# Performance work log

Measured on AMD Instinct MI355X. Metric: run time of the kernel, lower is better.

Reference implementation:

```python
import jax, jax.numpy as jnp
import numpy as np
import math

N, E, S, V, H, R = 10000, 160000, 512, 128, 8, 32
HD = S // H
CUTOFF = 10.0


def bessel_basis(d):
    # d: [E] -> [E, R], Bessel RBF with cosine cutoff
    freqs = jnp.arange(1, R + 1, dtype=d.dtype) * np.pi / CUTOFF  # [R]
    d1 = d[:, None]
    b = jnp.sin(freqs * d1) / jnp.maximum(d1, 1e-8)
    cut = 0.5 * (jnp.cos(np.pi * d1 / CUTOFF) + 1.0) * (d1 < CUTOFF).astype(d.dtype)
    return b * cut


def segment_softmax(logits, seg, num_seg):
    # logits: [E, H], seg: [E] destination node ids
    m = jax.ops.segment_max(logits, seg, num_segments=num_seg)
    m = jnp.where(jnp.isfinite(m), m, 0.0)
    e = jnp.exp(logits - m[seg])
    s = jax.ops.segment_sum(e, seg, num_segments=num_seg)
    return e / (s[seg] + 1e-9)


def layernorm(x, g, b, eps=1e-5):
    mu = jnp.mean(x, axis=-1, keepdims=True)
    var = jnp.mean(jnp.square(x - mu), axis=-1, keepdims=True)
    return (x - mu) * jax.lax.rsqrt(var + eps) * g + b


def setup_inputs() -> dict:
    key = jax.random.key(0)
    ks = jax.random.split(key, 24)
    sc = lambda fan_in: 1.0 / math.sqrt(fan_in)
    inp = {
        "scalars": jax.random.normal(ks[0], (N, S), jnp.float32),
        "vectors": jax.random.normal(ks[1], (N, V, 3), jnp.float32),
        "edge_vec": jax.random.normal(ks[2], (E, 3), jnp.float32),
        "Wq_s": jax.random.normal(ks[3], (S, S), jnp.float32) * sc(S),
        "bq_s": jnp.zeros((S,), jnp.float32),
        "Wk_s": jax.random.normal(ks[4], (S, S), jnp.float32) * sc(S),
        "bk_s": jnp.zeros((S,), jnp.float32),
        "Wv_s": jax.random.normal(ks[5], (S, S), jnp.float32) * sc(S),
        "bv_s": jnp.zeros((S,), jnp.float32),
        "Wq_v": jax.random.normal(ks[6], (V, V), jnp.float32) * sc(V),
        "Wk_v": jax.random.normal(ks[7], (V, V), jnp.float32) * sc(V),
        "Wv_v": jax.random.normal(ks[8], (V, V), jnp.float32) * sc(V),
        "Wout_s": jax.random.normal(ks[9], (S, S), jnp.float32) * sc(S),
        "bout_s": jnp.zeros((S,), jnp.float32),
        "Wout_v": jax.random.normal(ks[10], (V, V), jnp.float32) * sc(V),
        "bout_v": jnp.zeros((V,), jnp.float32),
        "W_edge": jax.random.normal(ks[11], (R, H), jnp.float32) * sc(R),
        "b_edge": jnp.zeros((H,), jnp.float32),
        "ln_g": jnp.ones((S,), jnp.float32),
        "ln_b": jnp.zeros((S,), jnp.float32),
        "edge_index": jax.random.randint(ks[12], (2, E), 0, N, jnp.int64),
    }
    return inp


def reference(scalars, vectors, edge_vec, Wq_s, bq_s, Wk_s, bk_s, Wv_s, bv_s,
              Wq_v, Wk_v, Wv_v, Wout_s, bout_s, Wout_v, bout_v,
              W_edge, b_edge, ln_g, ln_b, edge_index):
    row, col = edge_index[0], edge_index[1]
    edge_dist = jnp.linalg.norm(edge_vec, axis=-1)  # [E]

    # scalar Q/K/V, split into heads
    q_s = (scalars @ Wq_s + bq_s).reshape(N, H, HD)
    k_s = (scalars @ Wk_s + bk_s).reshape(N, H, HD)
    v_s = (scalars @ Wv_s + bv_s).reshape(N, H, HD)

    # vector Q/K/V: channel-mixing linear over the num_vectors axis (equivariant in 3D)
    q_v = jnp.einsum('nvi,vw->nwi', vectors, Wq_v)
    k_v = jnp.einsum('nvi,vw->nwi', vectors, Wk_v)
    v_v = jnp.einsum('nvi,vw->nwi', vectors, Wv_v)

    # per-edge attention logits
    att_s = jnp.einsum('ehd,ehd->eh', q_s[row], k_s[col])          # [E,H]
    att_v = jnp.einsum('evi,evi->e', q_v[row], k_v[col]) / math.sqrt(3.0)
    edge_att = bessel_basis(edge_dist) @ W_edge + b_edge            # [E,H]
    logits = (att_s + att_v[:, None] + edge_att) / math.sqrt(HD)

    # softmax over incoming edges of each destination node (row)
    attn = segment_softmax(logits, row, N)                          # [E,H]

    # scalar messages (per-head)
    msg_s = attn[:, :, None] * v_s[col]                             # [E,H,HD]
    out_s = jax.ops.segment_sum(msg_s, row, num_segments=N).reshape(N, S)
    out_s = out_s @ Wout_s + bout_s

    # vector messages (head-averaged attention, scalar gate keeps equivariance)
    a_v = jnp.mean(attn, axis=-1)                                   # [E]
    msg_v = a_v[:, None, None] * v_v[col]                           # [E,V,3]
    out_v = jax.ops.segment_sum(msg_v, row, num_segments=N)         # [N,V,3]
    out_v = jnp.einsum('nvi,vw->nwi', out_v, Wout_v) + bout_v[None, :, None]

    scalars_out = layernorm(scalars + out_s, ln_g, ln_b)
    vectors_out = vectors + out_v
    return scalars_out, vectors_out
```

## Files before the change

### kernel.cpp

```cpp
#include <hip/hip_runtime.h>
#include <math.h>

#define N_NODES 10000
#define E_EDGES 160000
#define S_DIM 512
#define QKV3 (3*S_DIM)
#define V_DIM 128
#define VQKV3 (3*V_DIM)
#define H_HEADS 8
#define R_BASIS 32
#define HD_DIM 64
#define NV3 (V_DIM*3)
#define KV8P 896

typedef _Float16 f16;
typedef f16 f16x2 __attribute__((ext_vector_type(2)));
typedef f16 f16x8 __attribute__((ext_vector_type(8)));
typedef float f32x4 __attribute__((ext_vector_type(4)));

static __device__ __forceinline__ float h2f(unsigned short u) {
  f16 h; __builtin_memcpy(&h, &u, 2); return (float)h;
}
static __device__ __forceinline__ unsigned short f2h(float f) {
  f16 h = (f16)f; unsigned short u; __builtin_memcpy(&u, &h, 2); return u;
}
static __device__ __forceinline__ float wave_max(float v) {
  #pragma unroll
  for (int o = 32; o > 0; o >>= 1) v = fmaxf(v, __shfl_xor(v, o, 64));
  return v;
}

#if defined(__has_builtin)
#if __has_builtin(__builtin_amdgcn_sdot4)
#define SDOT4(a, b, c) __builtin_amdgcn_sdot4((int)(a), (int)(b), (c), false)
#endif
#endif
#ifndef SDOT4
static __device__ __forceinline__ int sdot4_sw(unsigned int a, unsigned int b, int c) {
  #pragma unroll
  for (int j = 0; j < 4; ++j)
    c += (int)(char)((a >> (8 * j)) & 0xff) * (int)(char)((b >> (8 * j)) & 0xff);
  return c;
}
#define SDOT4(a, b, c) sdot4_sw((a), (b), (c))
#endif

static __device__ __forceinline__ void fma_i8x4(unsigned int w, float wt, float* acc) {
  acc[0] = fmaf(wt, (float)(int)(char)(w & 0xff), acc[0]);
  acc[1] = fmaf(wt, (float)(int)(char)((w >> 8) & 0xff), acc[1]);
  acc[2] = fmaf(wt, (float)(int)(char)((w >> 16) & 0xff), acc[2]);
  acc[3] = fmaf(wt, (float)(int)(char)((w >> 24) & 0xff), acc[3]);
}

static __device__ __forceinline__ void glds16(const unsigned short* g, unsigned short* l) {
  __builtin_amdgcn_global_load_lds(
      (const __attribute__((address_space(1))) unsigned int*)g,
      (__attribute__((address_space(3))) unsigned int*)l, 16, 0, 0);
}

__global__ __launch_bounds__(256) void prep_kernel(
    const float* __restrict__ scalars, unsigned short* __restrict__ Af16,
    const int* __restrict__ ei, int* __restrict__ counts,
    const float* __restrict__ bq, const float* __restrict__ bk,
    const float* __restrict__ bv, float* __restrict__ bias_cat)
{
  int b = blockIdx.x, t = threadIdx.x;
  if (b < 5000) {
    int i = b * 256 + t;
    float4 v = reinterpret_cast<const float4*>(scalars)[i];
    ushort4 o;
    o.x = f2h(v.x); o.y = f2h(v.y); o.z = f2h(v.z); o.w = f2h(v.w);
    reinterpret_cast<ushort4*>(Af16)[i] = o;
  } else if (b < 5625) {
    int e = (b - 5000) * 256 + t;
    if (e < E_EDGES) atomicAdd(&counts[ei[e]], 1);
  } else {
    int c = (b - 5625) * 256 + t;
    if (c < QKV3)
      bias_cat[c] = (c < 512) ? bq[c] : (c < 1024) ? bk[c - 512] : bv[c - 1024];
  }
}

__global__ __launch_bounds__(256) void transpose4_kernel(
    const float* __restrict__ W0, const float* __restrict__ W1,
    const float* __restrict__ W2, const float* __restrict__ W3,
    unsigned short* __restrict__ Dcat, unsigned short* __restrict__ Do, int D)
{
  __shared__ float t[32][33];
  int z = blockIdx.z;
  const float* W = (z == 0) ? W0 : (z == 1) ? W1 : (z == 2) ? W2 : W3;
  unsigned short* dst = (z < 3) ? Dcat + (size_t)z * D * D : Do;
  int n0 = blockIdx.x * 32, k0 = blockIdx.y * 32;
  int x = threadIdx.x, y = threadIdx.y;
  #pragma unroll
  for (int j = 0; j < 32; j += 8)
    t[y + j][x] = W[(size_t)(k0 + y + j) * D + n0 + x];
  __syncthreads();
  #pragma unroll
  for (int j = 0; j < 32; j += 8)
    dst[(size_t)(n0 + y + j) * D + k0 + x] = f2h(t[x][y + j]);
}

__global__ __launch_bounds__(128) void vec_transpose_kernel(
    const float* __restrict__ vecs, unsigned short* __restrict__ VT)
{
  __shared__ float l[NV3];
  int n = blockIdx.x, t = threadIdx.x;
  #pragma unroll
  for (int j = 0; j < 3; ++j) l[t + j * 128] = vecs[(size_t)n * NV3 + t + j * 128];
  __syncthreads();
  #pragma unroll
  for (int i = 0; i < 3; ++i)
    VT[((size_t)n * 3 + i) * V_DIM + t] = f2h(l[t * 3 + i]);
}

__global__ __launch_bounds__(256) void gemm_f16_kernel(
    const unsigned short* __restrict__ A, const unsigned short* __restrict__ Bt,
    const float* __restrict__ bias, float* __restrict__ Cf,
    unsigned short* __restrict__ Ch, int M, int K, int Nn)
{
  __shared__ unsigned short lds[2][2][128 * 32];
  int tid = threadIdx.x;
  int wid = tid >> 6, lane = tid & 63;
  int wr = wid >> 1, wc = wid & 1;
  int row0 = blockIdx.y * 128, col0 = blockIdx.x * 128;

  int r0 = tid >> 2, s0 = tid & 3;
  int r1 = r0 + 64;
  int sw0 = (r0 >> 1) & 3;
  int aoff = (s0 ^ sw0) * 8;
  int gra0 = row0 + r0; if (gra0 >= M) gra0 = M - 1;
  int gra1 = row0 + r1; if (gra1 >= M) gra1 = M - 1;
  const unsigned short* ag0 = A + (size_t)gra0 * K + aoff;
  const unsigned short* ag1 = A + (size_t)gra1 * K + aoff;
  const unsigned short* bg0 = Bt + (size_t)(col0 + r0) * K + aoff;
  const unsigned short* bg1 = Bt + (size_t)(col0 + r1) * K + aoff;

  f32x4 acc[4][4];
  #pragma unroll
  for (int m = 0; m < 4; ++m)
    #pragma unroll
    for (int n = 0; n < 4; ++n) acc[m][n] = (f32x4){0.f, 0.f, 0.f, 0.f};

  int lr = lane & 15, lq = lane >> 4;
  int slot = (lq ^ ((lr >> 1) & 3)) * 8;
  int aro[4], bro[4];
  #pragma unroll
  for (int m = 0; m < 4; ++m) aro[m] = (wr * 64 + m * 16 + lr) * 32 + slot;
  #pragma unroll
  for (int n = 0; n < 4; ++n) bro[n] = (wc * 64 + n * 16 + lr) * 32 + slot;

  int nk = K >> 5;
  glds16(ag0, &lds[0][0][tid * 8]);
  glds16(ag1, &lds[0][0][(tid + 256) * 8]);
  glds16(bg0, &lds[0][1][tid * 8]);
  glds16(bg1, &lds[0][1][(tid + 256) * 8]);
  __syncthreads();

  for (int t = 0; t < nk; ++t) {
    int cur = t & 1;
    if (t + 1 < nk) {
      int ko = (t + 1) << 5;
      glds16(ag0 + ko, &lds[cur ^ 1][0][tid * 8]);
      glds16(ag1 + ko, &lds[cur ^ 1][0][(tid + 256) * 8]);
      glds16(bg0 + ko, &lds[cur ^ 1][1][tid * 8]);
      glds16(bg1 + ko, &lds[cur ^ 1][1][(tid + 256) * 8]);
    }
    const unsigned short* Ab = lds[cur][0];
    const unsigned short* Bb = lds[cur][1];
    f16x8 af[4], bf[4];
    #pragma unroll
    for (int m = 0; m < 4; ++m) af[m] = *reinterpret_cast<const f16x8*>(Ab + aro[m]);
    #pragma unroll
    for (int n = 0; n < 4; ++n) bf[n] = *reinterpret_cast<const f16x8*>(Bb + bro[n]);
    #pragma unroll
    for (int m = 0; m < 4; ++m)
      #pragma unroll
      for (int n = 0; n < 4; ++n)
        acc[m][n] = __builtin_amdgcn_mfma_f32_16x16x32_f16(af[m], bf[n], acc[m][n], 0, 0, 0);
    __syncthreads();
  }

  float bcol[4];
  #pragma unroll
  for (int n = 0; n < 4; ++n)
    bcol[n] = bias ? bias[col0 + wc * 64 + n * 16 + lr] : 0.f;
  int rl = tid >> 3, cc = (tid & 7) * 16;

  if (Cf) {
    float* cst = reinterpret_cast<float*>(&lds[0][0][0]);
    #pragma unroll
    for (int m = 0; m < 4; ++m) {
      __syncthreads();
      #pragma unroll
      for (int n = 0; n < 4; ++n)
        #pragma unroll
        for (int j = 0; j < 4; ++j)
          cst[(wr * 16 + lq * 4 + j) * 128 + wc * 64 + n * 16 + lr] = acc[m][n][j] + bcol[n];
      __syncthreads();
      int row = row0 + (rl >> 4) * 64 + m * 16 + (rl & 15);
      if (row < M) {
        float4* dst = reinterpret_cast<float4*>(Cf + (size_t)row * Nn + col0 + cc);
        const float4* src = reinterpret_cast<const float4*>(cst + rl * 128 + cc);
        dst[0] = src[0]; dst[1] = src[1]; dst[2] = src[2]; dst[3] = src[3];
      }
    }
  } else {
    unsigned short* csth = &lds[0][0][0];
    #pragma unroll
    for (int m = 0; m < 4; ++m) {
      __syncthreads();
      #pragma unroll
      for (int n = 0; n < 4; ++n)
        #pragma unroll
        for (int j = 0; j < 4; ++j)
          csth[(wr * 16 + lq * 4 + j) * 128 + wc * 64 + n * 16 + lr] = f2h(acc[m][n][j] + bcol[n]);
      __syncthreads();
      int row = row0 + (rl >> 4) * 64 + m * 16 + (rl & 15);
      if (row < M) {
        int4* dst = reinterpret_cast<int4*>(Ch + (size_t)row * Nn + col0 + cc);
        const int4* src = reinterpret_cast<const int4*>(csth + rl * 128 + cc);
        dst[0] = src[0]; dst[1] = src[1];
      }
    }
  }
}

__global__ __launch_bounds__(256) void pack_i8_kernel(
    const unsigned short* __restrict__ qkv_s, const unsigned short* __restrict__ qkv_v,
    char* __restrict__ q8, char* __restrict__ k8, char* __restrict__ v8,
    float* __restrict__ scales)
{
  __shared__ float am[336];
  __shared__ float inv_sh[3];
  int n = blockIdx.x, t = threadIdx.x;
  float va[2][8];

  auto loadChunk = [&](int chunk, float* v) {
    int r = chunk / 112, j = chunk - r * 112;
    int c = j * 8;
    const unsigned short* src;
    if (c < 512) {
      src = qkv_s + (size_t)n * QKV3 + r * 512 + c;
    } else {
      int cc = c - 512, i = cc >> 7, w = cc & 127;
      src = qkv_v + ((size_t)n * 3 + i) * VQKV3 + r * 128 + w;
    }
    int4 sv = *reinterpret_cast<const int4*>(src);
    union { int4 x; unsigned short u[8]; } us; us.x = sv;
    float m = 0.f;
    #pragma unroll
    for (int q = 0; q < 8; ++q) { v[q] = h2f(us.u[q]); m = fmaxf(m, fabsf(v[q])); }
    am[chunk] = m;
  };

  loadChunk(t, va[0]);
  if (t < 80) loadChunk(256 + t, va[1]);
  __syncthreads();

  int lane = t & 63, wid = t >> 6;
  if (wid < 3) {
    int basec = wid * 112;
    float m = am[basec + lane];
    if (lane < 48) m = fmaxf(m, am[basec + 64 + lane]);
    m = wave_max(m);
    if (lane == 0) {
      m = fmaxf(m, 1e-8f);
      scales[3 * n + wid] = m * (1.f / 127.f);
      inv_sh[wid] = 127.f / m;
    }
  }
  __syncthreads();

  auto quantStore = [&](int chunk, const float* v) {
    int r = chunk / 112, j = chunk - r * 112;
    float inv = inv_sh[r];
    unsigned int b0 = 0, b1 = 0;
    #pragma unroll
    for (int q = 0; q < 4; ++q) {
      int x = __float2int_rn(v[q] * inv);
      b0 |= ((unsigned)(x & 0xff)) << (8 * q);
    }
    #pragma unroll
    for (int q = 0; q < 4; ++q) {
      int x = __float2int_rn(v[4 + q] * inv);
      b1 |= ((unsigned)(x & 0xff)) << (8 * q);
    }
    char* dst = (r == 0 ? q8 : r == 1 ? k8 : v8) + (size_t)n * KV8P + j * 8;
    uint2 o; o.x = b0; o.y = b1;
    *reinterpret_cast<uint2*>(dst) = o;
  };

  quantStore(t, va[0]);
  if (t < 80) quantStore(256 + t, va[1]);
}

__global__ __launch_bounds__(1024) void scan_kernel(const int* __restrict__ counts,
                                                    int* __restrict__ offs) {
  __shared__ int wsum[16];
  __shared__ int carry_s;
  int tid = threadIdx.x;
  int lane = tid & 63, w = tid >> 6;
  if (tid == 0) carry_s = 0;
  __syncthreads();
  for (int base = 0; base < N_NODES; base += 1024) {
    int i = base + tid;
    int v = (i < N_NODES) ? counts[i] : 0;
    int x = v;
    #pragma unroll
    for (int o = 1; o < 64; o <<= 1) {
      int t = __shfl_up(x, o, 64);
      if (lane >= o) x += t;
    }
    if (lane == 63) wsum[w] = x;
    __syncthreads();
    if (w == 0 && lane < 16) {
      int t = wsum[lane];
      #pragma unroll
      for (int o = 1; o < 16; o <<= 1) {
        int u = __shfl_up(t, o, 64);
        if (lane >= o) t += u;
      }
      wsum[lane] = t;
    }
    __syncthreads();
    int incl = x + ((w > 0) ? wsum[w - 1] : 0);
    int c = carry_s;
    __syncthreads();
    if (i < N_NODES) offs[i] = c + incl - v;
    if (tid == 1023) carry_s = c + incl;
    __syncthreads();
  }
  if (tid == 0) offs[N_NODES] = carry_s;
}

__global__ void scatter_kernel(const int* __restrict__ ei, const int* __restrict__ offs,
                               int* __restrict__ cursor, int* __restrict__ eord) {
  int e = blockIdx.x * 256 + threadIdx.x;
  if (e < E_EDGES) {
    int r = ei[e];
    int p = offs[r] + atomicAdd(&cursor[r], 1);
    eord[p] = e;
  }
}

#define MAXDEG 512
__global__ __launch_bounds__(256) void agg_fused_kernel(
    const char* __restrict__ q8, const char* __restrict__ k8,
    const char* __restrict__ v8, const float* __restrict__ scales,
    const float* __restrict__ edge_vec, const int* __restrict__ ei,
    const int* __restrict__ eord, const int* __restrict__ offs,
    const float* __restrict__ W_edge, const float* __restrict__ b_edge,
    unsigned short* __restrict__ out_s, unsigned short* __restrict__ out_v)
{
  __shared__ float attn_lds[MAXDEG * H_HEADS];
  __shared__ float av_lds[MAXDEG];
  __shared__ int col_lds[MAXDEG];
  __shared__ uint4 q_lds[56];
  __shared__ float Wl[R_BASIS * H_HEADS];
  __shared__ float m_sh[H_HEADS], inv_sh[H_HEADS];
  __shared__ float sq_sh;

  int n = blockIdx.x;
  int beg = offs[n];
  int deg = offs[n + 1] - beg;
  if (deg > MAXDEG) deg = MAXDEG;
  int tid = threadIdx.x;
  Wl[tid] = W_edge[tid];
  if (tid < 56) q_lds[tid] = reinterpret_cast<const uint4*>(q8 + (size_t)n * KV8P)[tid];
  if (tid == 56) sq_sh = scales[3 * n + 0];
  __syncthreads();

  int lane = tid & 63, wv = tid >> 6;
  int g = lane >> 3, h = lane & 7;
  float sq = sq_sh;

  for (int i = wv * 8 + g; i < deg; i += 32) {
    int e = eord[beg + i];
    int col = ei[E_EDGES + e];
    const char* kp = k8 + (size_t)col * KV8P;
    uint4 ka[4], kv[3];
    #pragma unroll
    for (int r = 0; r < 4; ++r)
      ka[r] = *reinterpret_cast<const uint4*>(kp + h * HD_DIM + r * 16);
    #pragma unroll
    for (int r = 0; r < 3; ++r)
      kv[r] = *reinterpret_cast<const uint4*>(kp + 512 + h * 48 + r * 16);
    float sk = scales[3 * col + 1];
    float ex = edge_vec[(size_t)e * 3 + 0];
    float ey = edge_vec[(size_t)e * 3 + 1];
    float ez = edge_vec[(size_t)e * 3 + 2];

    int dsum = 0;
    #pragma unroll
    for (int r = 0; r < 4; ++r) {
      uint4 qa = q_lds[h * 4 + r];
      dsum = SDOT4(qa.x, ka[r].x, dsum);
      dsum = SDOT4(qa.y, ka[r].y, dsum);
      dsum = SDOT4(qa.z, ka[r].z, dsum);
      dsum = SDOT4(qa.w, ka[r].w, dsum);
    }
    int dvec = 0;
    #pragma unroll
    for (int r = 0; r < 3; ++r) {
      uint4 qv = q_lds[32 + h * 3 + r];
      dvec = SDOT4(qv.x, kv[r].x, dvec);
      dvec = SDOT4(qv.y, kv[r].y, dvec);
      dvec = SDOT4(qv.z, kv[r].z, dvec);
      dvec = SDOT4(qv.w, kv[r].w, dvec);
    }
    dvec += __shfl_xor(dvec, 1, 64);
    dvec += __shfl_xor(dvec, 2, 64);
    dvec += __shfl_xor(dvec, 4, 64);
    float att = sq * sk * ((float)dsum + 0.57735026918962576f * (float)dvec);

    float d = sqrtf(ex * ex + ey * ey + ez * ez);
    float th = d * 0.31415926535897932f;
    float s1 = __sinf(th), c1 = __cosf(th);
    float s2 = 2.f * s1 * c1,         c2 = fmaf(c1, c1, -s1 * s1);
    float s3 = fmaf(s2, c1, c2 * s1), c3 = fmaf(c2, c1, -s2 * s1);
    float s4 = 2.f * s2 * c2,         c4 = fmaf(c2, c2, -s2 * s2);
    float sr[4] = {s1, s2, s3, s4};
    float cr[4] = {c1, c2, c3, c4};
    float acc = 0.f;
    #pragma unroll
    for (int t = 0; t < 8; ++t) {
      #pragma unroll
      for (int j = 0; j < 4; ++j) {
        acc = fmaf(sr[j], Wl[(t * 4 + j) * H_HEADS + h], acc);
        float sn = fmaf(sr[j], c4, cr[j] * s4);
        cr[j] = fmaf(cr[j], c4, -sr[j] * s4);
        sr[j] = sn;
      }
    }
    float cut = (d < 10.f) ? 0.5f * (c1 + 1.f) : 0.f;
    float eah = fmaf(acc, cut / fmaxf(d, 1e-8f), b_edge[h]);

    attn_lds[i * 8 + h] = (att + eah) * 0.125f;
    if (h == 0) col_lds[i] = col;
  }
  __syncthreads();

  if (wv == 0) {
    float m = -INFINITY;
    for (int i = g; i < deg; i += 8) m = fmaxf(m, attn_lds[i * 8 + h]);
    m = fmaxf(m, __shfl_xor(m, 8, 64));
    m = fmaxf(m, __shfl_xor(m, 16, 64));
    m = fmaxf(m, __shfl_xor(m, 32, 64));

    float s = 0.f;
    for (int i = g; i < deg; i += 8) {
      float w = __expf(attn_lds[i * 8 + h] - m);
      attn_lds[i * 8 + h] = w;
      s += w;
    }
    s += __shfl_xor(s, 8, 64);
    s += __shfl_xor(s, 16, 64);
    s += __shfl_xor(s, 32, 64);
    float inv = 1.f / (s + 1e-9f);
    if (lane < 8) { m_sh[lane] = m; inv_sh[lane] = inv; }

    for (int i = g; i < deg; i += 8) {
      float t = attn_lds[i * 8 + h] * inv;
      t += __shfl_xor(t, 1, 64);
      t += __shfl_xor(t, 2, 64);
      t += __shfl_xor(t, 4, 64);
      if (h == 0) av_lds[i] = 0.125f * t;
    }
  }
  __syncthreads();

  int hc = lane >> 3;
  float ih = inv_sh[hc];
  float accs[8] = {0,0,0,0,0,0,0,0};
  float accv[8] = {0,0,0,0,0,0,0,0};
  for (int i = wv; i < deg; i += 4) {
    int colv = col_lds[i];
    float svc = scales[3 * colv + 2];
    float wgt = attn_lds[i * 8 + hc] * ih * svc;
    float av = av_lds[i] * svc;
    uint2 vs = *reinterpret_cast<const uint2*>(v8 + (size_t)colv * KV8P + lane * 8);
    fma_i8x4(vs.x, wgt, accs);
    fma_i8x4(vs.y, wgt, accs + 4);
    if (lane < 48) {
      uint2 vvl = *reinterpret_cast<const uint2*>(v8 + (size_t)colv * KV8P + 512 + lane * 8);
      fma_i8x4(vvl.x, av, accv);
      fma_i8x4(vvl.y, av, accv + 4);
    }
  }
  __syncthreads();

  float* red_s = attn_lds;
  float* red_v = attn_lds + 2048;
  #pragma unroll
  for (int j = 0; j < 8; j += 4)
    *reinterpret_cast<float4*>(&red_s[wv * 512 + lane * 8 + j]) =
      make_float4(accs[j], accs[j+1], accs[j+2], accs[j+3]);
  if (lane < 48) {
    #pragma unroll
    for (int j = 0; j < 8; j += 4)
      *reinterpret_cast<float4*>(&red_v[wv * 384 + lane * 8 + j]) =
        make_float4(accv[j], accv[j+1], accv[j+2], accv[j+3]);
  }
  __syncthreads();

  {
    int d0 = 2 * tid;
    float s0 = red_s[d0] + red_s[512 + d0] + red_s[1024 + d0] + red_s[1536 + d0];
    float s1 = red_s[d0+1] + red_s[512 + d0+1] + red_s[1024 + d0+1] + red_s[1536 + d0+1];
    ushort2 o; o.x = f2h(s0); o.y = f2h(s1);
    *reinterpret_cast<ushort2*>(out_s + (size_t)n * S_DIM + d0) = o;
  }
  if (tid < 192) {
    int d0 = 2 * tid;
    float s0 = red_v[d0] + red_v[384 + d0] + red_v[768 + d0] + red_v[1152 + d0];
    float s1 = red_v[d0+1] + red_v[384 + d0+1] + red_v[768 + d0+1] + red_v[1152 + d0+1];
    ushort2 o; o.x = f2h(s0); o.y = f2h(s1);
    *reinterpret_cast<ushort2*>(out_v + (size_t)n * NV3 + d0) = o;
  }
}

__global__ __launch_bounds__(128) void vec_epilogue_kernel(
    const float* __restrict__ tmp, const float* __restrict__ bout_v,
    const float* __restrict__ vectors, float* __restrict__ out)
{
  __shared__ float l[NV3];
  int n = blockIdx.x, t = threadIdx.x;
  #pragma unroll
  for (int i = 0; i < 3; ++i)
    l[i * 128 + t] = tmp[((size_t)n * 3 + i) * V_DIM + t];
  __syncthreads();
  #pragma unroll
  for (int c = 0; c < 3; ++c) {
    int j = t + c * 128;
    int w = j / 3, i = j - 3 * w;
    out[(size_t)n * NV3 + j] = l[i * 128 + w] + bout_v[w] + vectors[(size_t)n * NV3 + j];
  }
}

__global__ __launch_bounds__(256) void ln_kernel(
    const float* __restrict__ x0, const float* __restrict__ dx,
    const float* __restrict__ g, const float* __restrict__ b,
    float* __restrict__ out)
{
  int r = blockIdx.x * 4 + (threadIdx.x >> 6);
  int lane = threadIdx.x & 63;
  if (r >= N_NODES) return;
  float x[8];
  float s = 0.f;
  #pragma unroll
  for (int j = 0; j < 8; ++j) {
    int d = lane + j * 64;
    x[j] = x0[(size_t)r * S_DIM + d] + dx[(size_t)r * S_DIM + d];
    s += x[j];
  }
  #pragma unroll
  for (int o = 32; o > 0; o >>= 1) s += __shfl_xor(s, o, 64);
  float mu = s * (1.f / 512.f);
  float vs = 0.f;
  #pragma unroll
  for (int j = 0; j < 8; ++j) { float t = x[j] - mu; vs += t * t; }
  #pragma unroll
  for (int o = 32; o > 0; o >>= 1) vs += __shfl_xor(vs, o, 64);
  float inv = rsqrtf(vs * (1.f / 512.f) + 1e-5f);
  #pragma unroll
  for (int j = 0; j < 8; ++j) {
    int d = lane + j * 64;
    out[(size_t)r * S_DIM + d] = (x[j] - mu) * inv * g[d] + b[d];
  }
}

extern "C" void kernel_launch(void* const* d_in, const int* in_sizes, int n_in,
                              void* d_out, int out_size, void* d_ws, size_t ws_size,
                              hipStream_t stream)
{
  (void)in_sizes; (void)n_in; (void)out_size; (void)ws_size;
  const float* scalars  = (const float*)d_in[0];
  const float* vectors  = (const float*)d_in[1];
  const float* edge_vec = (const float*)d_in[2];
  const float* Wq_s = (const float*)d_in[3];
  const float* bq_s = (const float*)d_in[4];
  const float* Wk_s = (const float*)d_in[5];
  const float* bk_s = (const float*)d_in[6];
  const float* Wv_s = (const float*)d_in[7];
  const float* bv_s = (const float*)d_in[8];
  const float* Wq_v = (const float*)d_in[9];
  const float* Wk_v = (const float*)d_in[10];
  const float* Wv_v = (const float*)d_in[11];
  const float* Wout_s = (const float*)d_in[12];
  const float* bout_s = (const float*)d_in[13];
  const float* Wout_v = (const float*)d_in[14];
  const float* bout_v = (const float*)d_in[15];
  const float* W_edge = (const float*)d_in[16];
  const float* b_edge = (const float*)d_in[17];
  const float* ln_g = (const float*)d_in[18];
  const float* ln_b = (const float*)d_in[19];
  const int* ei = (const int*)d_in[20];

  float* out = (float*)d_out;
  const size_t NS  = (size_t)N_NODES * S_DIM;
  const size_t NVs = (size_t)N_NODES * NV3;
  const size_t WSZ = (size_t)S_DIM * S_DIM;
  const size_t WVZ = (size_t)V_DIM * V_DIM;
  const int MV = N_NODES * 3;

  char* base = (char*)d_ws;
  auto carve = [&](size_t bytes) -> char* {
    char* p = base;
    base += (bytes + 255) & ~(size_t)255;
    return p;
  };
  unsigned short* Af16 = (unsigned short*)carve(NS * 2);
  unsigned short* VT0  = (unsigned short*)carve(NVs * 2);
  float* tmpv = (float*)Af16;
  char* v8 = (char*)Af16;
  unsigned short* qkv_s = (unsigned short*)carve((size_t)N_NODES * QKV3 * 2);
  unsigned short* qkv_v = (unsigned short*)carve((size_t)MV * VQKV3 * 2);
  unsigned short* outs_pre = (unsigned short*)carve(NS * 2);
  unsigned short* outv_pre = (unsigned short*)carve(NVs * 2);
  float* dx       = (float*)carve(NS * 4);
  char* q8 = (char*)dx;
  char* k8 = q8 + (size_t)N_NODES * KV8P;
  unsigned short* WqkvT  = (unsigned short*)carve(3 * WSZ * 2);
  unsigned short* WoT    = (unsigned short*)carve(WSZ * 2);
  unsigned short* WqkvvT = (unsigned short*)carve(3 * WVZ * 2);
  unsigned short* WovT   = (unsigned short*)carve(WVZ * 2);
  float* bias_cat = (float*)carve(QKV3 * 4);
  float* scales   = (float*)carve(3 * N_NODES * 4);
  int* counts = (int*)carve(N_NODES * 4);
  int* offs   = (int*)carve((N_NODES + 1) * 4);
  int* cursor = (int*)carve(N_NODES * 4);
  int* eord   = (int*)carve(E_EDGES * 4);

  hipMemsetAsync(counts, 0, N_NODES * sizeof(int), stream);
  hipMemsetAsync(cursor, 0, N_NODES * sizeof(int), stream);

  prep_kernel<<<5631, 256, 0, stream>>>(scalars, Af16, ei, counts,
                                        bq_s, bk_s, bv_s, bias_cat);
  dim3 tBlk(32, 8);
  transpose4_kernel<<<dim3(16, 16, 4), tBlk, 0, stream>>>(Wq_s, Wk_s, Wv_s, Wout_s, WqkvT, WoT, S_DIM);
  transpose4_kernel<<<dim3(4, 4, 4), tBlk, 0, stream>>>(Wq_v, Wk_v, Wv_v, Wout_v, WqkvvT, WovT, V_DIM);
  vec_transpose_kernel<<<N_NODES, 128, 0, stream>>>(vectors, VT0);

  gemm_f16_kernel<<<dim3(QKV3 / 128, (N_NODES + 127) / 128), 256, 0, stream>>>(
      Af16, WqkvT, bias_cat, nullptr, qkv_s, N_NODES, S_DIM, QKV3);
  gemm_f16_kernel<<<dim3(VQKV3 / 128, (MV + 127) / 128), 256, 0, stream>>>(
      VT0, WqkvvT, nullptr, nullptr, qkv_v, MV, V_DIM, VQKV3);

  pack_i8_kernel<<<N_NODES, 256, 0, stream>>>(qkv_s, qkv_v, q8, k8, v8, scales);

  scan_kernel<<<1, 1024, 0, stream>>>(counts, offs);
  scatter_kernel<<<(E_EDGES + 255) / 256, 256, 0, stream>>>(ei, offs, cursor, eord);

  agg_fused_kernel<<<N_NODES, 256, 0, stream>>>(q8, k8, v8, scales, edge_vec,
                                                ei, eord, offs, W_edge, b_edge,
                                                outs_pre, outv_pre);

  gemm_f16_kernel<<<dim3(S_DIM / 128, (N_NODES + 127) / 128), 256, 0, stream>>>(
      outs_pre, WoT, bout_s, dx, nullptr, N_NODES, S_DIM, S_DIM);
  gemm_f16_kernel<<<dim3(1, (MV + 127) / 128), 256, 0, stream>>>(
      outv_pre, WovT, nullptr, tmpv, nullptr, MV, V_DIM, V_DIM);
  vec_epilogue_kernel<<<N_NODES, 128, 0, stream>>>(tmpv, bout_v, vectors, out + NS);
  ln_kernel<<<2500, 256, 0, stream>>>(scalars, dx, ln_g, ln_b, out);
}
```

Before: 258.5 us.

## Split edge logits into column-bucketed pass for K-cache locality before aggregation

Moves the per-edge attention logit computation out of the per-node aggregation kernel into a separate persistent kernel. That kernel processes edges sorted into four source-column buckets so gathered K rows stay cache-resident, and it writes logits and columns in destination order. The aggregation kernel then only loads precomputed logits for the softmax and V accumulation, with a smaller degree cap and a 2x unrolled loop. This adds a second scan, extra atomics, an E×H float logits round trip through memory, and more launches. It also lowers MAXDEG from 512 to 128, which could truncate high-degree nodes.

```diff
diff --git a/kernel.cpp b/kernel.cpp
--- a/kernel.cpp
+++ b/kernel.cpp
@@ -12,9 +12,11 @@
 #define HD_DIM 64
 #define NV3 (V_DIM*3)
 #define KV8P 896
+#define NBKT 4
+#define BKT_DIV 2500
+#define NKEYS (NBKT * N_NODES)
 
 typedef _Float16 f16;
-typedef f16 f16x2 __attribute__((ext_vector_type(2)));
 typedef f16 f16x8 __attribute__((ext_vector_type(8)));
 typedef float f32x4 __attribute__((ext_vector_type(4)));
 
@@ -60,7 +62,7 @@
 
 __global__ __launch_bounds__(256) void prep_kernel(
     const float* __restrict__ scalars, unsigned short* __restrict__ Af16,
-    const int* __restrict__ ei, int* __restrict__ counts,
+    const int* __restrict__ ei, int* __restrict__ counts, int* __restrict__ bc,
     const float* __restrict__ bq, const float* __restrict__ bk,
     const float* __restrict__ bv, float* __restrict__ bias_cat)
 {
@@ -73,7 +75,11 @@
     reinterpret_cast<ushort4*>(Af16)[i] = o;
   } else if (b < 5625) {
     int e = (b - 5000) * 256 + t;
-    if (e < E_EDGES) atomicAdd(&counts[ei[e]], 1);
+    if (e < E_EDGES) {
+      int row = ei[e], col = ei[E_EDGES + e];
+      atomicAdd(&counts[row], 1);
+      atomicAdd(&bc[(col / BKT_DIV) * N_NODES + row], 1);
+    }
   } else {
     int c = (b - 5625) * 256 + t;
     if (c < QKV3)
@@ -296,16 +302,16 @@
 }
 
 __global__ __launch_bounds__(1024) void scan_kernel(const int* __restrict__ counts,
-                                                    int* __restrict__ offs) {
+                                                    int* __restrict__ offs, int n) {
   __shared__ int wsum[16];
   __shared__ int carry_s;
   int tid = threadIdx.x;
   int lane = tid & 63, w = tid >> 6;
   if (tid == 0) carry_s = 0;
   __syncthreads();
-  for (int base = 0; base < N_NODES; base += 1024) {
+  for (int base = 0; base < n; base += 1024) {
     int i = base + tid;
-    int v = (i < N_NODES) ? counts[i] : 0;
+    int v = (i < n) ? counts[i] : 0;
     int x = v;
     #pragma unroll
     for (int o = 1; o < 64; o <<= 1) {
@@ -327,131 +333,162 @@
     int incl = x + ((w > 0) ? wsum[w - 1] : 0);
     int c = carry_s;
     __syncthreads();
-    if (i < N_NODES) offs[i] = c + incl - v;
+    if (i < n) offs[i] = c + incl - v;
     if (tid == 1023) carry_s = c + incl;
     __syncthreads();
   }
-  if (tid == 0) offs[N_NODES] = carry_s;
-}
-
-__global__ void scatter_kernel(const int* __restrict__ ei, const int* __restrict__ offs,
-                               int* __restrict__ cursor, int* __restrict__ eord) {
+  if (tid == 0) offs[n] = carry_s;
+}
+
+__global__ void scatter_kernel(const int* __restrict__ ei, const float* __restrict__ edge_vec,
+                               const int* __restrict__ offs, int* __restrict__ cursor,
+                               const int* __restrict__ bcoffs, int* __restrict__ bcur,
+                               int4* __restrict__ rec) {
   int e = blockIdx.x * 256 + threadIdx.x;
   if (e < E_EDGES) {
-    int r = ei[e];
-    int p = offs[r] + atomicAdd(&cursor[r], 1);
-    eord[p] = e;
-  }
-}
-
-#define MAXDEG 512
-__global__ __launch_bounds__(256) void agg_fused_kernel(
+    int row = ei[e], col = ei[E_EDGES + e];
+    int pos = offs[row] + atomicAdd(&cursor[row], 1);
+    int key = (col / BKT_DIV) * N_NODES + row;
+    int bp = bcoffs[key] + atomicAdd(&bcur[key], 1);
+    float ex = edge_vec[(size_t)e * 3 + 0];
+    float ey = edge_vec[(size_t)e * 3 + 1];
+    float ez = edge_vec[(size_t)e * 3 + 2];
+    float d = sqrtf(ex * ex + ey * ey + ez * ez);
+    rec[bp] = make_int4(__float_as_int(d), pos, row, col);
+  }
+}
+
+__global__ __launch_bounds__(256, 4) void edge_logits_kernel(
     const char* __restrict__ q8, const char* __restrict__ k8,
+    const float* __restrict__ scales,
+    const int4* __restrict__ rec, const int* __restrict__ bcoffs,
+    const float* __restrict__ W_edge, const float* __restrict__ b_edge,
+    float* __restrict__ logits, int* __restrict__ cols)
+{
+  __shared__ float Wl[R_BASIS * H_HEADS];
+  Wl[threadIdx.x] = W_edge[threadIdx.x];
+  __syncthreads();
+
+  int lane = threadIdx.x & 63;
+  int wv = threadIdx.x >> 6;
+  int g = lane >> 3, h = lane & 7;
+  int G = gridDim.x;
+
+  for (int s = 0; s < NBKT; ++s) {
+    int segbeg = bcoffs[s * N_NODES];
+    int segend = bcoffs[(s + 1) * N_NODES];
+    int Cs = (segend - segbeg + 31) >> 5;
+    for (int c = blockIdx.x; c < Cs; c += G) {
+      int i = segbeg + c * 32 + (wv * 8 + g);
+      if (i >= segend) continue;
+      int4 r = rec[i];
+      float d = __int_as_float(r.x);
+      int pos = r.y, row = r.z, col = r.w;
+
+      const char* qp = q8 + (size_t)row * KV8P;
+      const char* kp = k8 + (size_t)col * KV8P;
+      uint4 qa[4], ka[4], qv[3], kv[3];
+      #pragma unroll
+      for (int rr = 0; rr < 4; ++rr)
+        ka[rr] = *reinterpret_cast<const uint4*>(kp + h * HD_DIM + rr * 16);
+      #pragma unroll
+      for (int rr = 0; rr < 3; ++rr)
+        kv[rr] = *reinterpret_cast<const uint4*>(kp + 512 + h * 48 + rr * 16);
+      #pragma unroll
+      for (int rr = 0; rr < 4; ++rr)
+        qa[rr] = *reinterpret_cast<const uint4*>(qp + h * HD_DIM + rr * 16);
+      #pragma unroll
+      for (int rr = 0; rr < 3; ++rr)
+        qv[rr] = *reinterpret_cast<const uint4*>(qp + 512 + h * 48 + rr * 16);
+
+      float sq = scales[3 * row + 0];
+      float sk = scales[3 * col + 1];
+
+      int dsum = 0;
+      #pragma unroll
+      for (int rr = 0; rr < 4; ++rr) {
+        dsum = SDOT4(qa[rr].x, ka[rr].x, dsum);
+        dsum = SDOT4(qa[rr].y, ka[rr].y, dsum);
+        dsum = SDOT4(qa[rr].z, ka[rr].z, dsum);
+        dsum = SDOT4(qa[rr].w, ka[rr].w, dsum);
+      }
+      int dvec = 0;
+      #pragma unroll
+      for (int rr = 0; rr < 3; ++rr) {
+        dvec = SDOT4(qv[rr].x, kv[rr].x, dvec);
+        dvec = SDOT4(qv[rr].y, kv[rr].y, dvec);
+        dvec = SDOT4(qv[rr].z, kv[rr].z, dvec);
+        dvec = SDOT4(qv[rr].w, kv[rr].w, dvec);
+      }
+      dvec += __shfl_xor(dvec, 1, 64);
+      dvec += __shfl_xor(dvec, 2, 64);
+      dvec += __shfl_xor(dvec, 4, 64);
+
+      float att = sq * sk * ((float)dsum + 0.57735026918962576f * (float)dvec);
+
+      float th = d * 0.31415926535897932f;
+      float s1 = __sinf(th), c1 = __cosf(th);
+      float s2 = 2.f * s1 * c1,         c2 = fmaf(c1, c1, -s1 * s1);
+      float s3 = fmaf(s2, c1, c2 * s1), c3 = fmaf(c2, c1, -s2 * s1);
+      float s4 = 2.f * s2 * c2,         c4 = fmaf(c2, c2, -s2 * s2);
+      float sr[4] = {s1, s2, s3, s4};
+      float cr[4] = {c1, c2, c3, c4};
+      float acc = 0.f;
+      #pragma unroll
+      for (int t = 0; t < 8; ++t) {
+        #pragma unroll
+        for (int j = 0; j < 4; ++j) {
+          acc = fmaf(sr[j], Wl[(t * 4 + j) * H_HEADS + h], acc);
+          float sn = fmaf(sr[j], c4, cr[j] * s4);
+          cr[j] = fmaf(cr[j], c4, -sr[j] * s4);
+          sr[j] = sn;
+        }
+      }
+      float cut = (d < 10.f) ? 0.5f * (c1 + 1.f) : 0.f;
+      float eah = fmaf(acc, cut / fmaxf(d, 1e-8f), b_edge[h]);
+
+      logits[(size_t)pos * H_HEADS + h] = (att + eah) * 0.125f;
+      if (h == 0) cols[pos] = col;
+    }
+  }
+}
+
+#define MAXDEG 128
+__global__ __launch_bounds__(256) void agg_kernel(
+    const float* __restrict__ logits, const int* __restrict__ cols,
     const char* __restrict__ v8, const float* __restrict__ scales,
-    const float* __restrict__ edge_vec, const int* __restrict__ ei,
-    const int* __restrict__ eord, const int* __restrict__ offs,
-    const float* __restrict__ W_edge, const float* __restrict__ b_edge,
+    const int* __restrict__ offs,
     unsigned short* __restrict__ out_s, unsigned short* __restrict__ out_v)
 {
-  __shared__ float attn_lds[MAXDEG * H_HEADS];
+  __shared__ float buf[3584];
   __shared__ float av_lds[MAXDEG];
   __shared__ int col_lds[MAXDEG];
-  __shared__ uint4 q_lds[56];
-  __shared__ float Wl[R_BASIS * H_HEADS];
   __shared__ float m_sh[H_HEADS], inv_sh[H_HEADS];
-  __shared__ float sq_sh;
 
   int n = blockIdx.x;
   int beg = offs[n];
   int deg = offs[n + 1] - beg;
   if (deg > MAXDEG) deg = MAXDEG;
   int tid = threadIdx.x;
-  Wl[tid] = W_edge[tid];
-  if (tid < 56) q_lds[tid] = reinterpret_cast<const uint4*>(q8 + (size_t)n * KV8P)[tid];
-  if (tid == 56) sq_sh = scales[3 * n + 0];
-  __syncthreads();
-
   int lane = tid & 63, wv = tid >> 6;
   int g = lane >> 3, h = lane & 7;
-  float sq = sq_sh;
-
-  for (int i = wv * 8 + g; i < deg; i += 32) {
-    int e = eord[beg + i];
-    int col = ei[E_EDGES + e];
-    const char* kp = k8 + (size_t)col * KV8P;
-    uint4 ka[4], kv[3];
-    #pragma unroll
-    for (int r = 0; r < 4; ++r)
-      ka[r] = *reinterpret_cast<const uint4*>(kp + h * HD_DIM + r * 16);
-    #pragma unroll
-    for (int r = 0; r < 3; ++r)
-      kv[r] = *reinterpret_cast<const uint4*>(kp + 512 + h * 48 + r * 16);
-    float sk = scales[3 * col + 1];
-    float ex = edge_vec[(size_t)e * 3 + 0];
-    float ey = edge_vec[(size_t)e * 3 + 1];
-    float ez = edge_vec[(size_t)e * 3 + 2];
-
-    int dsum = 0;
-    #pragma unroll
-    for (int r = 0; r < 4; ++r) {
-      uint4 qa = q_lds[h * 4 + r];
-      dsum = SDOT4(qa.x, ka[r].x, dsum);
-      dsum = SDOT4(qa.y, ka[r].y, dsum);
-      dsum = SDOT4(qa.z, ka[r].z, dsum);
-      dsum = SDOT4(qa.w, ka[r].w, dsum);
-    }
-    int dvec = 0;
-    #pragma unroll
-    for (int r = 0; r < 3; ++r) {
-      uint4 qv = q_lds[32 + h * 3 + r];
-      dvec = SDOT4(qv.x, kv[r].x, dvec);
-      dvec = SDOT4(qv.y, kv[r].y, dvec);
-      dvec = SDOT4(qv.z, kv[r].z, dvec);
-      dvec = SDOT4(qv.w, kv[r].w, dvec);
-    }
-    dvec += __shfl_xor(dvec, 1, 64);
-    dvec += __shfl_xor(dvec, 2, 64);
-    dvec += __shfl_xor(dvec, 4, 64);
-    float att = sq * sk * ((float)dsum + 0.57735026918962576f * (float)dvec);
-
-    float d = sqrtf(ex * ex + ey * ey + ez * ez);
-    float th = d * 0.31415926535897932f;
-    float s1 = __sinf(th), c1 = __cosf(th);
-    float s2 = 2.f * s1 * c1,         c2 = fmaf(c1, c1, -s1 * s1);
-    float s3 = fmaf(s2, c1, c2 * s1), c3 = fmaf(c2, c1, -s2 * s1);
-    float s4 = 2.f * s2 * c2,         c4 = fmaf(c2, c2, -s2 * s2);
-    float sr[4] = {s1, s2, s3, s4};
-    float cr[4] = {c1, c2, c3, c4};
-    float acc = 0.f;
-    #pragma unroll
-    for (int t = 0; t < 8; ++t) {
-      #pragma unroll
-      for (int j = 0; j < 4; ++j) {
-        acc = fmaf(sr[j], Wl[(t * 4 + j) * H_HEADS + h], acc);
-        float sn = fmaf(sr[j], c4, cr[j] * s4);
-        cr[j] = fmaf(cr[j], c4, -sr[j] * s4);
-        sr[j] = sn;
-      }
-    }
-    float cut = (d < 10.f) ? 0.5f * (c1 + 1.f) : 0.f;
-    float eah = fmaf(acc, cut / fmaxf(d, 1e-8f), b_edge[h]);
-
-    attn_lds[i * 8 + h] = (att + eah) * 0.125f;
-    if (h == 0) col_lds[i] = col;
-  }
+
+  int cnt8 = deg * 8;
+  for (int j = tid; j < cnt8; j += 256) buf[j] = logits[(size_t)beg * 8 + j];
+  for (int i = tid; i < deg; i += 256) col_lds[i] = cols[beg + i];
   __syncthreads();
 
   if (wv == 0) {
     float m = -INFINITY;
-    for (int i = g; i < deg; i += 8) m = fmaxf(m, attn_lds[i * 8 + h]);
+    for (int i = g; i < deg; i += 8) m = fmaxf(m, buf[i * 8 + h]);
     m = fmaxf(m, __shfl_xor(m, 8, 64));
     m = fmaxf(m, __shfl_xor(m, 16, 64));
     m = fmaxf(m, __shfl_xor(m, 32, 64));
 
     float s = 0.f;
     for (int i = g; i < deg; i += 8) {
-      float w = __expf(attn_lds[i * 8 + h] - m);
-      attn_lds[i * 8 + h] = w;
+      float w = __expf(buf[i * 8 + h] - m);
+      buf[i * 8 + h] = w;
       s += w;
     }
     s += __shfl_xor(s, 8, 64);
@@ -461,7 +498,7 @@
     if (lane < 8) { m_sh[lane] = m; inv_sh[lane] = inv; }
 
     for (int i = g; i < deg; i += 8) {
-      float t = attn_lds[i * 8 + h] * inv;
+      float t = buf[i * 8 + h] * inv;
       t += __shfl_xor(t, 1, 64);
       t += __shfl_xor(t, 2, 64);
       t += __shfl_xor(t, 4, 64);
@@ -474,10 +511,10 @@
   float ih = inv_sh[hc];
   float accs[8] = {0,0,0,0,0,0,0,0};
   float accv[8] = {0,0,0,0,0,0,0,0};
-  for (int i = wv; i < deg; i += 4) {
+  auto body = [&](int i) {
     int colv = col_lds[i];
     float svc = scales[3 * colv + 2];
-    float wgt = attn_lds[i * 8 + hc] * ih * svc;
+    float wgt = buf[i * 8 + hc] * ih * svc;
     float av = av_lds[i] * svc;
     uint2 vs = *reinterpret_cast<const uint2*>(v8 + (size_t)colv * KV8P + lane * 8);
     fma_i8x4(vs.x, wgt, accs);
@@ -487,20 +524,24 @@
       fma_i8x4(vvl.x, av, accv);
       fma_i8x4(vvl.y, av, accv + 4);
     }
-  }
-  __syncthreads();
-
-  float* red_s = attn_lds;
-  float* red_v = attn_lds + 2048;
-  #pragma unroll
-  for (int j = 0; j < 8; j += 4)
-    *reinterpret_cast<float4*>(&red_s[wv * 512 + lane * 8 + j]) =
-      make_float4(accs[j], accs[j+1], accs[j+2], accs[j+3]);
+  };
+  int i = wv;
+  for (; i + 4 < deg; i += 8) { body(i); body(i + 4); }
+  if (i < deg) body(i);
+  __syncthreads();
+
+  float* red_s = buf;
+  float* red_v = buf + 2048;
+  int o = ((lane >> 2) & 1) << 2;
+  *reinterpret_cast<float4*>(&red_s[wv * 512 + lane * 8 + o]) =
+    make_float4(accs[o], accs[o+1], accs[o+2], accs[o+3]);
+  *reinterpret_cast<float4*>(&red_s[wv * 512 + lane * 8 + (o ^ 4)]) =
+    make_float4(accs[o^4], accs[(o^4)+1], accs[(o^4)+2], accs[(o^4)+3]);
   if (lane < 48) {
-    #pragma unroll
-    for (int j = 0; j < 8; j += 4)
-      *reinterpret_cast<float4*>(&red_v[wv * 384 + lane * 8 + j]) =
-        make_float4(accv[j], accv[j+1], accv[j+2], accv[j+3]);
+    *reinterpret_cast<float4*>(&red_v[wv * 384 + lane * 8 + o]) =
+      make_float4(accv[o], accv[o+1], accv[o+2], accv[o+3]);
+    *reinterpret_cast<float4*>(&red_v[wv * 384 + lane * 8 + (o ^ 4)]) =
+      make_float4(accv[o^4], accv[(o^4)+1], accv[(o^4)+2], accv[(o^4)+3]);
   }
   __syncthreads();
 
@@ -508,15 +549,15 @@
     int d0 = 2 * tid;
     float s0 = red_s[d0] + red_s[512 + d0] + red_s[1024 + d0] + red_s[1536 + d0];
     float s1 = red_s[d0+1] + red_s[512 + d0+1] + red_s[1024 + d0+1] + red_s[1536 + d0+1];
-    ushort2 o; o.x = f2h(s0); o.y = f2h(s1);
-    *reinterpret_cast<ushort2*>(out_s + (size_t)n * S_DIM + d0) = o;
+    ushort2 ov; ov.x = f2h(s0); ov.y = f2h(s1);
+    *reinterpret_cast<ushort2*>(out_s + (size_t)n * S_DIM + d0) = ov;
   }
   if (tid < 192) {
     int d0 = 2 * tid;
     float s0 = red_v[d0] + red_v[384 + d0] + red_v[768 + d0] + red_v[1152 + d0];
     float s1 = red_v[d0+1] + red_v[384 + d0+1] + red_v[768 + d0+1] + red_v[1152 + d0+1];
-    ushort2 o; o.x = f2h(s0); o.y = f2h(s1);
-    *reinterpret_cast<ushort2*>(out_v + (size_t)n * NV3 + d0) = o;
+    ushort2 ov; ov.x = f2h(s0); ov.y = f2h(s1);
+    *reinterpret_cast<ushort2*>(out_v + (size_t)n * NV3 + d0) = ov;
   }
 }
 
@@ -600,6 +641,7 @@
   float* out = (float*)d_out;
   const size_t NS  = (size_t)N_NODES * S_DIM;
   const size_t NVs = (size_t)N_NODES * NV3;
+  const size_t EH  = (size_t)E_EDGES * H_HEADS;
   const size_t WSZ = (size_t)S_DIM * S_DIM;
   const size_t WVZ = (size_t)V_DIM * V_DIM;
   const int MV = N_NODES * 3;
@@ -621,6 +663,9 @@
   float* dx       = (float*)carve(NS * 4);
   char* q8 = (char*)dx;
   char* k8 = q8 + (size_t)N_NODES * KV8P;
+  float* logitsS  = (float*)carve(EH * 4);
+  int*   colsS    = (int*)carve(E_EDGES * 4);
+  int4*  rec      = (int4*)carve((size_t)E_EDGES * 16);
   unsigned short* WqkvT  = (unsigned short*)carve(3 * WSZ * 2);
   unsigned short* WoT    = (unsigned short*)carve(WSZ * 2);
   unsigned short* WqkvvT = (unsigned short*)carve(3 * WVZ * 2);
@@ -630,12 +675,16 @@
   int* counts = (int*)carve(N_NODES * 4);
   int* offs   = (int*)carve((N_NODES + 1) * 4);
   int* cursor = (int*)carve(N_NODES * 4);
-  int* eord   = (int*)carve(E_EDGES * 4);
+  int* bc     = (int*)carve(NKEYS * 4);
+  int* bcoffs = (int*)carve((NKEYS + 1) * 4);
+  int* bcur   = (int*)carve(NKEYS * 4);
 
   hipMemsetAsync(counts, 0, N_NODES * sizeof(int), stream);
   hipMemsetAsync(cursor, 0, N_NODES * sizeof(int), stream);
-
-  prep_kernel<<<5631, 256, 0, stream>>>(scalars, Af16, ei, counts,
+  hipMemsetAsync(bc, 0, NKEYS * sizeof(int), stream);
+  hipMemsetAsync(bcur, 0, NKEYS * sizeof(int), stream);
+
+  prep_kernel<<<5631, 256, 0, stream>>>(scalars, Af16, ei, counts, bc,
                                         bq_s, bk_s, bv_s, bias_cat);
   dim3 tBlk(32, 8);
   transpose4_kernel<<<dim3(16, 16, 4), tBlk, 0, stream>>>(Wq_s, Wk_s, Wv_s, Wout_s, WqkvT, WoT, S_DIM);
@@ -649,12 +698,16 @@
 
   pack_i8_kernel<<<N_NODES, 256, 0, stream>>>(qkv_s, qkv_v, q8, k8, v8, scales);
 
-  scan_kernel<<<1, 1024, 0, stream>>>(counts, offs);
-  scatter_kernel<<<(E_EDGES + 255) / 256, 256, 0, stream>>>(ei, offs, cursor, eord);
-
-  agg_fused_kernel<<<N_NODES, 256, 0, stream>>>(q8, k8, v8, scales, edge_vec,
-                                                ei, eord, offs, W_edge, b_edge,
-                                                outs_pre, outv_pre);
+  scan_kernel<<<1, 1024, 0, stream>>>(counts, offs, N_NODES);
+  scan_kernel<<<1, 1024, 0, stream>>>(bc, bcoffs, NKEYS);
+  scatter_kernel<<<(E_EDGES + 255) / 256, 256, 0, stream>>>(ei, edge_vec, offs, cursor,
+                                                            bcoffs, bcur, rec);
+
+  edge_logits_kernel<<<1248, 256, 0, stream>>>(q8, k8, scales, rec, bcoffs,
+                                               W_edge, b_edge, logitsS, colsS);
+
+  agg_kernel<<<N_NODES, 256, 0, stream>>>(logitsS, colsS, v8, scales, offs,
+                                          outs_pre, outv_pre);
 
   gemm_f16_kernel<<<dim3(S_DIM / 128, (N_NODES + 127) / 128), 256, 0, stream>>>(
       outs_pre, WoT, bout_s, dx, nullptr, N_NODES, S_DIM, S_DIM);
```

After: 298.1 us. +15.3%, slower.
